# Kernel optimization log

Hardware: AMD Instinct MI355X
Metric: run time of the kernel (lower is better)

The kernel has to match this reference:

```python
import jax, jax.numpy as jnp
import numpy as np

EPS = 1e-5
NUM = 16  # number of per-prototype experts


def _layernorm(x, gamma, beta):
    # normalize over last dim; gamma/beta broadcast against x
    mu = jnp.mean(x, axis=-1, keepdims=True)
    var = jnp.var(x, axis=-1, keepdims=True)
    return (x - mu) * jax.lax.rsqrt(var + EPS) * gamma + beta


def setup_inputs() -> dict:
    key = jax.random.key(0)
    ks = jax.random.split(key, 6)
    B, P, D = 2048, 32, 1024
    s = 1.0 / np.sqrt(D)
    return {
        "x": jax.random.normal(ks[0], (B, P, D), dtype=jnp.float32),
        # per-prototype expert params (stacked over expert dim)
        "g_e": jnp.ones((NUM, D), jnp.float32),
        "b_e": jnp.zeros((NUM, D), jnp.float32),
        "W1_e": jax.random.normal(ks[1], (NUM, D, D), jnp.float32) * s,
        "b1_e": jnp.zeros((NUM, D), jnp.float32),
        "W2_e": jax.random.normal(ks[2], (NUM, D, D), jnp.float32) * s,
        "b2_e": jnp.zeros((NUM, D), jnp.float32),
        # shared MLP params for remaining prototypes
        "g_s": jnp.ones((D,), jnp.float32),
        "b_s": jnp.zeros((D,), jnp.float32),
        "W1_s": jax.random.normal(ks[3], (D, D), jnp.float32) * s,
        "b1_s": jnp.zeros((D,), jnp.float32),
        "W2_s": jax.random.normal(ks[4], (D, D), jnp.float32) * s,
        "b2_s": jnp.zeros((D,), jnp.float32),
    }


def reference(x, g_e, b_e, W1_e, b1_e, W2_e, b2_e,
              g_s, b_s, W1_s, b1_s, W2_s, b2_s):
    # x: (B, P, D); first NUM prototypes go through per-prototype experts,
    # the rest through a single shared MLP. Dropout p=0 => identity.
    xe = x[:, :NUM, :]                     # (B, NUM, D)
    y = _layernorm(xe, g_e, b_e)           # per-expert LN params broadcast over B
    h = jnp.einsum('bnd,ndh->bnh', y, W1_e) + b1_e
    h = jax.nn.gelu(h, approximate=False)  # torch nn.GELU default = exact erf
    out_e = jnp.einsum('bnh,nhk->bnk', h, W2_e) + b2_e

    xr = x[:, NUM:, :]                     # (B, P-NUM, D)
    yr = _layernorm(xr, g_s, b_s)
    hr = jax.nn.gelu(yr @ W1_s + b1_s, approximate=False)
    out_s = hr @ W2_s + b2_s

    return jnp.concatenate([out_e, out_s], axis=1)
```

## Files before the change

kernel.cpp:

```cpp
#include <hip/hip_runtime.h>
#include <hip/hip_bf16.h>
#include <cstdint>
#include <math.h>

using u16 = unsigned short;
typedef __attribute__((ext_vector_type(8))) short bf16x8;
typedef __attribute__((ext_vector_type(4))) float f32x4;

static __device__ __forceinline__ u16 f2bf(float f) {
    union { float f; unsigned int u; } v; v.f = f;
    return (u16)((v.u + 0x7FFFu + ((v.u >> 16) & 1u)) >> 16);
}

typedef const __attribute__((address_space(1))) unsigned int* gptr_t;
typedef __attribute__((address_space(3))) unsigned int* lptr_t;

static __device__ __forceinline__ void load_lds16(const void* g, void* l) {
    __builtin_amdgcn_global_load_lds((gptr_t)g, (lptr_t)l, 16, 0, 0);
}

static __device__ __forceinline__ void bar() {
    asm volatile("s_barrier" ::: "memory");
}

__global__ __launch_bounds__(256)
void wconv(const float* __restrict__ W1e, const float* __restrict__ W1s,
           const float* __restrict__ W2e, const float* __restrict__ W2s,
           u16* __restrict__ Wt)
{
    const int mat = blockIdx.z;
    const float* src;
    if (mat < 17) src = (mat < 16) ? (W1e + (size_t)mat * 1048576) : W1s;
    else {
        const int m2 = mat - 17;
        src = (m2 < 16) ? (W2e + (size_t)m2 * 1048576) : W2s;
    }
    u16* dst = Wt + (size_t)mat * 1048576;

    __shared__ float tile[32][33];
    const int tx = threadIdx.x & 31, ty = threadIdx.x >> 5;
    const int c0 = blockIdx.x * 32, r0 = blockIdx.y * 32;

#pragma unroll
    for (int j = 0; j < 32; j += 8)
        tile[ty + j][tx] = src[(size_t)(r0 + ty + j) * 1024 + c0 + tx];
    __syncthreads();
#pragma unroll
    for (int j = 0; j < 32; j += 8)
        dst[(size_t)(c0 + ty + j) * 1024 + r0 + tx] = f2bf(tile[tx][ty + j]);
}

__global__ __launch_bounds__(256)
void ln_kernel(const float* __restrict__ x,
               const float* __restrict__ g_e, const float* __restrict__ b_e,
               const float* __restrict__ g_s, const float* __restrict__ b_s,
               u16* __restrict__ Yg)
{
    const int row  = blockIdx.x * 4 + (threadIdx.x >> 6);
    const int lane = threadIdx.x & 63;
    const int b = row >> 5, p = row & 31;

    const float4* x4 = (const float4*)(x + (size_t)row * 1024) + lane * 4;
    float4 v[4];
    float sum = 0.f, ssq = 0.f;
#pragma unroll
    for (int i = 0; i < 4; i++) {
        v[i] = x4[i];
        sum += v[i].x + v[i].y + v[i].z + v[i].w;
        ssq += v[i].x * v[i].x + v[i].y * v[i].y + v[i].z * v[i].z + v[i].w * v[i].w;
    }
#pragma unroll
    for (int off = 32; off > 0; off >>= 1) {
        sum += __shfl_xor(sum, off);
        ssq += __shfl_xor(ssq, off);
    }
    const float mean = sum * (1.0f / 1024.0f);
    const float var  = ssq * (1.0f / 1024.0f) - mean * mean;
    const float rstd = rsqrtf(var + 1e-5f);

    const float4* g4 = (const float4*)((p < 16) ? (g_e + p * 1024) : g_s) + lane * 4;
    const float4* b4 = (const float4*)((p < 16) ? (b_e + p * 1024) : b_s) + lane * 4;

    __attribute__((aligned(16))) u16 o[16];
#pragma unroll
    for (int i = 0; i < 4; i++) {
        const float4 g = g4[i], bb = b4[i];
        o[i * 4 + 0] = f2bf((v[i].x - mean) * rstd * g.x + bb.x);
        o[i * 4 + 1] = f2bf((v[i].y - mean) * rstd * g.y + bb.y);
        o[i * 4 + 2] = f2bf((v[i].z - mean) * rstd * g.z + bb.z);
        o[i * 4 + 3] = f2bf((v[i].w - mean) * rstd * g.w + bb.w);
    }
    u16* dst = Yg + ((size_t)p * 2048 + b) * 1024 + lane * 16;
    ((uint4*)dst)[0] = ((const uint4*)o)[0];
    ((uint4*)dst)[1] = ((const uint4*)o)[1];
}

static __device__ __forceinline__ void stage2(const u16* gb, u16* lb,
                                              const size_t* sg, const int* sl) {
    load_lds16(gb + sg[0], lb + sl[0]);
    load_lds16(gb + sg[1], lb + sl[1]);
}

static __device__ __forceinline__ bf16x8 ld_frag(const u16* h, int row, int slot) {
    return *(const bf16x8*)(h + row * 64 + slot * 8);
}

#define MFMA_BF16 __builtin_amdgcn_mfma_f32_16x16x32_bf16

template <int STAGE>
__global__ __launch_bounds__(512, 2)
void gemm_ffn(const u16* __restrict__ Abase, const u16* __restrict__ Wt,
              const float* __restrict__ bias_e, const float* __restrict__ bias_s,
              u16* __restrict__ Hout, float* __restrict__ Fout)
{
    const int d   = blockIdx.x;
    const int vid = (d & 7) * 128 + (d >> 3);
    const int p   = vid >> 5;
    const int rem = vid & 31;
    const int m0  = (rem >> 2) * 256;
    const int n0  = (rem & 3) * 256;

    const u16* Ap = Abase + (size_t)p * (2048u * 1024u);
    const u16* Bp = Wt + (size_t)((p < 16) ? p : 16) * (1024u * 1024u);
    const float* bias = (p < 16) ? (bias_e + p * 1024) : bias_s;

    __shared__ u16 lds[2][2][2][8192];

    const int tid = threadIdx.x;
    const int w = tid >> 6, l = tid & 63;
    const int lr = l & 15, kq = l >> 4;
    const int wmh = w >> 2;
    const int wq  = w & 3;
    const int wnh = wq >> 1;
    const int bnb = (wq & 1) * 64;
    const int sl0 = kq ^ (lr & 7);
    const int sl1 = sl0 ^ 4;

    size_t sg[2]; int slo[2];
#pragma unroll
    for (int j = 0; j < 2; j++) {
        const int g = tid + j * 512;
        const int r = g >> 3;
        const int c = (g & 7) ^ (r & 7);
        sg[j]  = (size_t)r * 1024 + c * 8;
        slo[j] = g * 8;
    }

    f32x4 acc[8][4];
#pragma unroll
    for (int i = 0; i < 8; i++)
#pragma unroll
        for (int j = 0; j < 4; j++)
            acc[i][j] = (f32x4){0.f, 0.f, 0.f, 0.f};

    stage2(Ap + (size_t)(m0      ) * 1024,      &lds[0][0][0][0], sg, slo);
    stage2(Ap + (size_t)(m0 + 128) * 1024,      &lds[0][0][1][0], sg, slo);
    stage2(Bp + (size_t)(n0      ) * 1024,      &lds[0][1][0][0], sg, slo);
    stage2(Bp + (size_t)(n0 + 128) * 1024,      &lds[0][1][1][0], sg, slo);
    stage2(Bp + (size_t)(n0      ) * 1024 + 64, &lds[1][1][0][0], sg, slo);
    stage2(Bp + (size_t)(n0 + 128) * 1024 + 64, &lds[1][1][1][0], sg, slo);
    asm volatile("s_waitcnt vmcnt(4)" ::: "memory");
    bar();

    bf16x8 a[4][2], b[4][2];

    for (int t = 0; t < 16; ++t) {
        const int sl = t & 1, ot = sl ^ 1;
        const u16* hA = &lds[sl][0][wmh][0];
        const u16* hB = &lds[sl][1][wnh][0];

#pragma unroll
        for (int i = 0; i < 4; ++i) {
            a[i][0] = ld_frag(hA, i * 16 + lr, sl0);
            a[i][1] = ld_frag(hA, i * 16 + lr, sl1);
        }
#pragma unroll
        for (int j = 0; j < 2; ++j) {
            b[j][0] = ld_frag(hB, bnb + j * 16 + lr, sl0);
            b[j][1] = ld_frag(hB, bnb + j * 16 + lr, sl1);
        }
        if (t < 15)
            stage2(Ap + (size_t)m0 * 1024 + (t + 1) * 64, &lds[ot][0][0][0], sg, slo);
        bar();
        __builtin_amdgcn_s_setprio(1);
#pragma unroll
        for (int i = 0; i < 4; ++i)
#pragma unroll
            for (int j = 0; j < 2; ++j) {
                acc[i][j] = MFMA_BF16(a[i][0], b[j][0], acc[i][j], 0, 0, 0);
                acc[i][j] = MFMA_BF16(a[i][1], b[j][1], acc[i][j], 0, 0, 0);
            }
        __builtin_amdgcn_s_setprio(0);
        bar();

#pragma unroll
        for (int j = 0; j < 2; ++j) {
            b[2 + j][0] = ld_frag(hB, bnb + (2 + j) * 16 + lr, sl0);
            b[2 + j][1] = ld_frag(hB, bnb + (2 + j) * 16 + lr, sl1);
        }
        if (t < 15)
            stage2(Ap + (size_t)(m0 + 128) * 1024 + (t + 1) * 64, &lds[ot][0][1][0], sg, slo);
        bar();
        __builtin_amdgcn_s_setprio(1);
#pragma unroll
        for (int i = 0; i < 4; ++i)
#pragma unroll
            for (int j = 0; j < 2; ++j) {
                acc[i][2 + j] = MFMA_BF16(a[i][0], b[2 + j][0], acc[i][2 + j], 0, 0, 0);
                acc[i][2 + j] = MFMA_BF16(a[i][1], b[2 + j][1], acc[i][2 + j], 0, 0, 0);
            }
        __builtin_amdgcn_s_setprio(0);
        bar();

#pragma unroll
        for (int i = 0; i < 4; ++i) {
            a[i][0] = ld_frag(hA, (4 + i) * 16 + lr, sl0);
            a[i][1] = ld_frag(hA, (4 + i) * 16 + lr, sl1);
        }
        if (t < 14)
            stage2(Bp + (size_t)n0 * 1024 + (t + 2) * 64, &lds[sl][1][0][0], sg, slo);
        bar();
        __builtin_amdgcn_s_setprio(1);
#pragma unroll
        for (int i = 0; i < 4; ++i)
#pragma unroll
            for (int j = 0; j < 2; ++j) {
                acc[4 + i][j] = MFMA_BF16(a[i][0], b[j][0], acc[4 + i][j], 0, 0, 0);
                acc[4 + i][j] = MFMA_BF16(a[i][1], b[j][1], acc[4 + i][j], 0, 0, 0);
            }
        __builtin_amdgcn_s_setprio(0);
        bar();

        if (t < 14)
            stage2(Bp + (size_t)(n0 + 128) * 1024 + (t + 2) * 64, &lds[sl][1][1][0], sg, slo);
        bar();
        __builtin_amdgcn_s_setprio(1);
#pragma unroll
        for (int i = 0; i < 4; ++i)
#pragma unroll
            for (int j = 0; j < 2; ++j) {
                acc[4 + i][2 + j] = MFMA_BF16(a[i][0], b[2 + j][0], acc[4 + i][2 + j], 0, 0, 0);
                acc[4 + i][2 + j] = MFMA_BF16(a[i][1], b[2 + j][1], acc[4 + i][2 + j], 0, 0, 0);
            }
        __builtin_amdgcn_s_setprio(0);
        if (t < 14) asm volatile("s_waitcnt vmcnt(4)" ::: "memory");
        else        asm volatile("s_waitcnt vmcnt(0)" ::: "memory");
        bar();
    }

    float bv[4];
#pragma unroll
    for (int j = 0; j < 4; ++j) bv[j] = bias[n0 + wq * 64 + j * 16 + lr];

#pragma unroll
    for (int mi = 0; mi < 8; ++mi) {
        const int rbase = m0 + wmh * 128 + mi * 16 + kq * 4;
#pragma unroll
        for (int r = 0; r < 4; ++r) {
            const int row = rbase + r;
#pragma unroll
            for (int nj = 0; nj < 4; ++nj) {
                const int col = n0 + wq * 64 + nj * 16 + lr;
                float v2 = acc[mi][nj][r] + bv[nj];
                if (STAGE == 1) {
                    v2 = 0.5f * v2 * (1.0f + erff(v2 * 0.70710678118654752f));
                    Hout[(size_t)p * (2048u * 1024u) + (size_t)row * 1024 + col] = f2bf(v2);
                } else {
                    Fout[((size_t)row * 32 + p) * 1024 + col] = v2;
                }
            }
        }
    }
}

extern "C" void kernel_launch(void* const* d_in, const int* in_sizes, int n_in,
                              void* d_out, int out_size, void* d_ws, size_t ws_size,
                              hipStream_t stream)
{
    const float* x    = (const float*)d_in[0];
    const float* g_e  = (const float*)d_in[1];
    const float* b_e  = (const float*)d_in[2];
    const float* W1_e = (const float*)d_in[3];
    const float* b1_e = (const float*)d_in[4];
    const float* W2_e = (const float*)d_in[5];
    const float* b2_e = (const float*)d_in[6];
    const float* g_s  = (const float*)d_in[7];
    const float* b_s  = (const float*)d_in[8];
    const float* W1_s = (const float*)d_in[9];
    const float* b1_s = (const float*)d_in[10];
    const float* W2_s = (const float*)d_in[11];
    const float* b2_s = (const float*)d_in[12];
    float* out = (float*)d_out;

    u16* Wt = (u16*)d_ws;
    u16* Yg = Wt + (size_t)34 * 1024 * 1024;
    u16* Hg = Yg + (size_t)32 * 2048 * 1024;

    wconv<<<dim3(32, 32, 34), 256, 0, stream>>>(W1_e, W1_s, W2_e, W2_s, Wt);
    ln_kernel<<<16384, 256, 0, stream>>>(x, g_e, b_e, g_s, b_s, Yg);
    gemm_ffn<1><<<dim3(1024), 512, 0, stream>>>(Yg, Wt, b1_e, b1_s, Hg, nullptr);
    gemm_ffn<2><<<dim3(1024), 512, 0, stream>>>(Hg, Wt + (size_t)17 * 1024 * 1024,
                                                b2_e, b2_s, nullptr, out);
}
```

Baseline: 927.8 us.

## Merge weight conversion and layernorm into one prep kernel, pin GEMM barriers

Fuses the weight transpose/convert kernel and the layernorm kernel into a single launch that dispatches on block index. The transpose writes become 8-byte vector stores, and layernorm loads are re-indexed so consecutive lanes read consecutive float4s for coalescing. In the GEMM, barriers are wrapped with sched_barrier and an explicit lgkmcnt(0) wait is added before each MFMA phase, which stops the compiler from moving instructions across the barriers but may serialize LDS reads with compute.

Measured after the change: 887.7 us. -4.3%, faster.

```diff
diff --git a/kernel.cpp b/kernel.cpp
--- a/kernel.cpp
+++ b/kernel.cpp
@@ -6,6 +6,7 @@
 using u16 = unsigned short;
 typedef __attribute__((ext_vector_type(8))) short bf16x8;
 typedef __attribute__((ext_vector_type(4))) float f32x4;
+typedef __attribute__((ext_vector_type(4))) unsigned short u16x4;
 
 static __device__ __forceinline__ u16 f2bf(float f) {
     union { float f; unsigned int u; } v; v.f = f;
@@ -19,80 +20,88 @@
     __builtin_amdgcn_global_load_lds((gptr_t)g, (lptr_t)l, 16, 0, 0);
 }
 
-static __device__ __forceinline__ void bar() {
+static __device__ __forceinline__ void bar_pin() {
+    __builtin_amdgcn_sched_barrier(0);
     asm volatile("s_barrier" ::: "memory");
+    __builtin_amdgcn_sched_barrier(0);
+}
+static __device__ __forceinline__ void wait_lds0() {
+    asm volatile("s_waitcnt lgkmcnt(0)" ::: "memory");
+    __builtin_amdgcn_sched_barrier(0);
 }
 
 __global__ __launch_bounds__(256)
-void wconv(const float* __restrict__ W1e, const float* __restrict__ W1s,
-           const float* __restrict__ W2e, const float* __restrict__ W2s,
-           u16* __restrict__ Wt)
+void prep(const float* __restrict__ W1e, const float* __restrict__ W1s,
+          const float* __restrict__ W2e, const float* __restrict__ W2s,
+          const float* __restrict__ x,
+          const float* __restrict__ g_e, const float* __restrict__ b_e,
+          const float* __restrict__ g_s, const float* __restrict__ b_s,
+          u16* __restrict__ Wt, u16* __restrict__ Yg)
 {
-    const int mat = blockIdx.z;
-    const float* src;
-    if (mat < 17) src = (mat < 16) ? (W1e + (size_t)mat * 1048576) : W1s;
-    else {
-        const int m2 = mat - 17;
-        src = (m2 < 16) ? (W2e + (size_t)m2 * 1048576) : W2s;
+    const int id = blockIdx.x;
+    if (id < 34816) {
+        const int mat = id >> 10;
+        const int rr  = id & 1023;
+        const int c0  = (rr & 31) * 32, r0 = (rr >> 5) * 32;
+        const float* src;
+        if (mat < 17) src = (mat < 16) ? (W1e + (size_t)mat * 1048576) : W1s;
+        else {
+            const int m2 = mat - 17;
+            src = (m2 < 16) ? (W2e + (size_t)m2 * 1048576) : W2s;
+        }
+        u16* dst = Wt + (size_t)mat * 1048576;
+
+        __shared__ float tile[32][33];
+        const int tx = threadIdx.x & 31, ty = threadIdx.x >> 5;
+#pragma unroll
+        for (int j = 0; j < 32; j += 8)
+            tile[ty + j][tx] = src[(size_t)(r0 + ty + j) * 1024 + c0 + tx];
+        __syncthreads();
+
+        const int q  = threadIdx.x & 7;
+        const int oc = threadIdx.x >> 3;
+        u16x4 o4;
+#pragma unroll
+        for (int j = 0; j < 4; j++) o4[j] = f2bf(tile[q * 4 + j][oc]);
+        *(u16x4*)(dst + (size_t)(c0 + oc) * 1024 + r0 + q * 4) = o4;
+    } else {
+        const int row  = (id - 34816) * 4 + (threadIdx.x >> 6);
+        const int lane = threadIdx.x & 63;
+        const int b = row >> 5, p = row & 31;
+
+        const float4* x4 = (const float4*)(x + (size_t)row * 1024);
+        float4 v[4];
+        float sum = 0.f, ssq = 0.f;
+#pragma unroll
+        for (int i = 0; i < 4; i++) {
+            v[i] = x4[lane + 64 * i];
+            sum += v[i].x + v[i].y + v[i].z + v[i].w;
+            ssq += v[i].x * v[i].x + v[i].y * v[i].y + v[i].z * v[i].z + v[i].w * v[i].w;
+        }
+#pragma unroll
+        for (int off = 32; off > 0; off >>= 1) {
+            sum += __shfl_xor(sum, off);
+            ssq += __shfl_xor(ssq, off);
+        }
+        const float mean = sum * (1.0f / 1024.0f);
+        const float var  = ssq * (1.0f / 1024.0f) - mean * mean;
+        const float rstd = rsqrtf(var + 1e-5f);
+
+        const float4* g4 = (const float4*)((p < 16) ? (g_e + p * 1024) : g_s);
+        const float4* b4 = (const float4*)((p < 16) ? (b_e + p * 1024) : b_s);
+        u16* dst = Yg + ((size_t)p * 2048 + b) * 1024;
+
+#pragma unroll
+        for (int i = 0; i < 4; i++) {
+            const float4 g = g4[lane + 64 * i], bb = b4[lane + 64 * i];
+            u16x4 o;
+            o[0] = f2bf((v[i].x - mean) * rstd * g.x + bb.x);
+            o[1] = f2bf((v[i].y - mean) * rstd * g.y + bb.y);
+            o[2] = f2bf((v[i].z - mean) * rstd * g.z + bb.z);
+            o[3] = f2bf((v[i].w - mean) * rstd * g.w + bb.w);
+            *(u16x4*)(dst + lane * 4 + i * 256) = o;
+        }
     }
-    u16* dst = Wt + (size_t)mat * 1048576;
-
-    __shared__ float tile[32][33];
-    const int tx = threadIdx.x & 31, ty = threadIdx.x >> 5;
-    const int c0 = blockIdx.x * 32, r0 = blockIdx.y * 32;
-
-#pragma unroll
-    for (int j = 0; j < 32; j += 8)
-        tile[ty + j][tx] = src[(size_t)(r0 + ty + j) * 1024 + c0 + tx];
-    __syncthreads();
-#pragma unroll
-    for (int j = 0; j < 32; j += 8)
-        dst[(size_t)(c0 + ty + j) * 1024 + r0 + tx] = f2bf(tile[tx][ty + j]);
-}
-
-__global__ __launch_bounds__(256)
-void ln_kernel(const float* __restrict__ x,
-               const float* __restrict__ g_e, const float* __restrict__ b_e,
-               const float* __restrict__ g_s, const float* __restrict__ b_s,
-               u16* __restrict__ Yg)
-{
-    const int row  = blockIdx.x * 4 + (threadIdx.x >> 6);
-    const int lane = threadIdx.x & 63;
-    const int b = row >> 5, p = row & 31;
-
-    const float4* x4 = (const float4*)(x + (size_t)row * 1024) + lane * 4;
-    float4 v[4];
-    float sum = 0.f, ssq = 0.f;
-#pragma unroll
-    for (int i = 0; i < 4; i++) {
-        v[i] = x4[i];
-        sum += v[i].x + v[i].y + v[i].z + v[i].w;
-        ssq += v[i].x * v[i].x + v[i].y * v[i].y + v[i].z * v[i].z + v[i].w * v[i].w;
-    }
-#pragma unroll
-    for (int off = 32; off > 0; off >>= 1) {
-        sum += __shfl_xor(sum, off);
-        ssq += __shfl_xor(ssq, off);
-    }
-    const float mean = sum * (1.0f / 1024.0f);
-    const float var  = ssq * (1.0f / 1024.0f) - mean * mean;
-    const float rstd = rsqrtf(var + 1e-5f);
-
-    const float4* g4 = (const float4*)((p < 16) ? (g_e + p * 1024) : g_s) + lane * 4;
-    const float4* b4 = (const float4*)((p < 16) ? (b_e + p * 1024) : b_s) + lane * 4;
-
-    __attribute__((aligned(16))) u16 o[16];
-#pragma unroll
-    for (int i = 0; i < 4; i++) {
-        const float4 g = g4[i], bb = b4[i];
-        o[i * 4 + 0] = f2bf((v[i].x - mean) * rstd * g.x + bb.x);
-        o[i * 4 + 1] = f2bf((v[i].y - mean) * rstd * g.y + bb.y);
-        o[i * 4 + 2] = f2bf((v[i].z - mean) * rstd * g.z + bb.z);
-        o[i * 4 + 3] = f2bf((v[i].w - mean) * rstd * g.w + bb.w);
-    }
-    u16* dst = Yg + ((size_t)p * 2048 + b) * 1024 + lane * 16;
-    ((uint4*)dst)[0] = ((const uint4*)o)[0];
-    ((uint4*)dst)[1] = ((const uint4*)o)[1];
 }
 
 static __device__ __forceinline__ void stage2(const u16* gb, u16* lb,
@@ -160,7 +169,7 @@
     stage2(Bp + (size_t)(n0      ) * 1024 + 64, &lds[1][1][0][0], sg, slo);
     stage2(Bp + (size_t)(n0 + 128) * 1024 + 64, &lds[1][1][1][0], sg, slo);
     asm volatile("s_waitcnt vmcnt(4)" ::: "memory");
-    bar();
+    bar_pin();
 
     bf16x8 a[4][2], b[4][2];
 
@@ -181,7 +190,8 @@
         }
         if (t < 15)
             stage2(Ap + (size_t)m0 * 1024 + (t + 1) * 64, &lds[ot][0][0][0], sg, slo);
-        bar();
+        bar_pin();
+        wait_lds0();
         __builtin_amdgcn_s_setprio(1);
 #pragma unroll
         for (int i = 0; i < 4; ++i)
@@ -191,7 +201,7 @@
                 acc[i][j] = MFMA_BF16(a[i][1], b[j][1], acc[i][j], 0, 0, 0);
             }
         __builtin_amdgcn_s_setprio(0);
-        bar();
+        bar_pin();
 
 #pragma unroll
         for (int j = 0; j < 2; ++j) {
@@ -200,7 +210,8 @@
         }
         if (t < 15)
             stage2(Ap + (size_t)(m0 + 128) * 1024 + (t + 1) * 64, &lds[ot][0][1][0], sg, slo);
-        bar();
+        bar_pin();
+        wait_lds0();
         __builtin_amdgcn_s_setprio(1);
 #pragma unroll
         for (int i = 0; i < 4; ++i)
@@ -210,7 +221,7 @@
                 acc[i][2 + j] = MFMA_BF16(a[i][1], b[2 + j][1], acc[i][2 + j], 0, 0, 0);
             }
         __builtin_amdgcn_s_setprio(0);
-        bar();
+        bar_pin();
 
 #pragma unroll
         for (int i = 0; i < 4; ++i) {
@@ -219,7 +230,8 @@
         }
         if (t < 14)
             stage2(Bp + (size_t)n0 * 1024 + (t + 2) * 64, &lds[sl][1][0][0], sg, slo);
-        bar();
+        bar_pin();
+        wait_lds0();
         __builtin_amdgcn_s_setprio(1);
 #pragma unroll
         for (int i = 0; i < 4; ++i)
@@ -229,11 +241,11 @@
                 acc[4 + i][j] = MFMA_BF16(a[i][1], b[j][1], acc[4 + i][j], 0, 0, 0);
             }
         __builtin_amdgcn_s_setprio(0);
-        bar();
+        bar_pin();
 
         if (t < 14)
             stage2(Bp + (size_t)(n0 + 128) * 1024 + (t + 2) * 64, &lds[sl][1][1][0], sg, slo);
-        bar();
+        bar_pin();
         __builtin_amdgcn_s_setprio(1);
 #pragma unroll
         for (int i = 0; i < 4; ++i)
@@ -245,7 +257,7 @@
         __builtin_amdgcn_s_setprio(0);
         if (t < 14) asm volatile("s_waitcnt vmcnt(4)" ::: "memory");
         else        asm volatile("s_waitcnt vmcnt(0)" ::: "memory");
-        bar();
+        bar_pin();
     }
 
     float bv[4];
@@ -296,8 +308,8 @@
     u16* Yg = Wt + (size_t)34 * 1024 * 1024;
     u16* Hg = Yg + (size_t)32 * 2048 * 1024;
 
-    wconv<<<dim3(32, 32, 34), 256, 0, stream>>>(W1_e, W1_s, W2_e, W2_s, Wt);
-    ln_kernel<<<16384, 256, 0, stream>>>(x, g_e, b_e, g_s, b_s, Yg);
+    prep<<<dim3(51200), 256, 0, stream>>>(W1_e, W1_s, W2_e, W2_s,
+                                          x, g_e, b_e, g_s, b_s, Wt, Yg);
     gemm_ffn<1><<<dim3(1024), 512, 0, stream>>>(Yg, Wt, b1_e, b1_s, Hg, nullptr);
     gemm_ffn<2><<<dim3(1024), 512, 0, stream>>>(Hg, Wt + (size_t)17 * 1024 * 1024,
                                                 b2_e, b2_s, nullptr, out);
```
